# Kernel optimization log

Hardware: AMD Instinct MI355X
Metric: run time of the kernel (lower is better)

Reference implementation:

```python
import jax, jax.numpy as jnp
import numpy as np
import math

N, CIN, DM, H, W = 4, 64, 32, 64, 64
KH = KW = 3

def setup_inputs() -> dict:
    key = jax.random.key(0)
    ks = jax.random.split(key, 12)
    sc = 0.05
    return {
        "h": jax.random.normal(ks[0], (N, CIN, H, W), jnp.float32),
        "m": jax.random.normal(ks[1], (N, CIN, H, W), jnp.float32),
        "Wh": jax.random.normal(ks[2], (3 * DM, CIN), jnp.float32) * sc,
        "bh": jax.random.normal(ks[3], (3 * DM,), jnp.float32) * sc,
        "Wm": jax.random.normal(ks[4], (2 * DM, CIN), jnp.float32) * sc,
        "bm": jax.random.normal(ks[5], (2 * DM,), jnp.float32) * sc,
        "Wz": jax.random.normal(ks[6], (DM, 2 * DM), jnp.float32) * sc,
        "bz": jax.random.normal(ks[7], (DM,), jnp.float32) * sc,
        "Wo": jax.random.normal(ks[8], (3 * CIN, CIN + DM, KH, KW), jnp.float32) * sc,
        "bo": jax.random.normal(ks[9], (3 * CIN,), jnp.float32) * sc,
    }

def _conv1x1(x, Wt, b):
    # x: [N,Ci,H,W], Wt: [Co,Ci] -> [N,Co,H,W]
    return jnp.einsum('oi,nihw->nohw', Wt, x) + b[None, :, None, None]

def _attend(q, k, v):
    # q,k,v: [N,C,S]; out: [N,C,S]
    C = q.shape[1]
    scores = jnp.einsum('ncs,nct->nst', q, k) / math.sqrt(C)  # [N,S,S]
    attn = jax.nn.softmax(scores, axis=-1)
    return jnp.einsum('nst,nct->ncs', attn, v)

def reference(h, m, Wh, bh, Wm, bm, Wz, bz, Wo, bo):
    n, _, hh, ww = h.shape
    S = hh * ww
    hq, hk, hv = jnp.split(_conv1x1(h, Wh, bh), 3, axis=1)
    mk, mv = jnp.split(_conv1x1(m, Wm, bm), 2, axis=1)
    hq = hq.reshape(n, DM, S)
    hk = hk.reshape(n, DM, S)
    hv = hv.reshape(n, DM, S)
    mk = mk.reshape(n, DM, S)
    mv = mv.reshape(n, DM, S)
    Zh = _attend(hq, hk, hv).reshape(n, DM, hh, ww)
    Zm = _attend(hq, mk, mv).reshape(n, DM, hh, ww)
    Z = _conv1x1(jnp.concatenate([Zh, Zm], axis=1), Wz, bz)
    x = jnp.concatenate([Z, h], axis=1)  # [N, DM+CIN, H, W]
    out = jax.lax.conv_general_dilated(
        x, Wo, window_strides=(1, 1), padding='SAME',
        dimension_numbers=('NCHW', 'OIHW', 'NCHW')) + bo[None, :, None, None]
    i, g, o = jnp.split(out, 3, axis=1)
    i = jax.nn.sigmoid(i)
    g = jnp.tanh(g)
    m_next = i * g + (1.0 - i) * m
    h_next = jax.nn.sigmoid(o) * m_next
    return (h_next, m_next)
```

## Files before the change

kernel.cpp:

```cpp
#include <hip/hip_runtime.h>
#include <math.h>

#define NB 4
#define CIN 64
#define DM 32
#define S 4096
#define NW 4

#define OFF_Q  0
#define OFF_KH 262144
#define OFF_VH 524288
#define OFF_KM 786432
#define OFF_VM 1048576
#define OFF_ZH 1310720
#define OFF_ZM 1572864
#define OFF_WF 1835008

typedef __attribute__((ext_vector_type(8))) short bf16x8;
typedef __attribute__((ext_vector_type(4))) short s16x4;
typedef __attribute__((ext_vector_type(4))) float f32x4;
typedef __attribute__((ext_vector_type(2))) unsigned int u32x2;

__device__ inline unsigned short f2b(float x) {
  union { float f; unsigned u; } v;
  v.f = x;
  unsigned r = (v.u + 0x7FFF + ((v.u >> 16) & 1)) >> 16;
  return (unsigned short)r;
}

__device__ inline float b2f(unsigned short u) {
  union { unsigned u; float f; } v;
  v.u = ((unsigned)u) << 16;
  return v.f;
}

__device__ inline unsigned fbits(float x) {
  union { float f; unsigned u; } v;
  v.f = x;
  return v.u;
}

__global__ __launch_bounds__(256) void prep_kernel(
    const float* __restrict__ h, const float* __restrict__ m,
    const float* __restrict__ Wh, const float* __restrict__ bh,
    const float* __restrict__ Wm, const float* __restrict__ bm,
    const float* __restrict__ Wo, float* __restrict__ ws) {
  __shared__ unsigned short sm[64][34];
  int bid = blockIdx.x;
  int tid = threadIdx.x;

  if (bid >= 512) {
    int idx = (bid - 512) * 256 + tid;
    int co = idx / 432;
    int rem = idx - co * 432;
    int tap = rem / 48;
    int cp = rem - tap * 48;
    int ci0 = cp * 2;
    float a = Wo[((size_t)co * 96 + ci0) * 9 + tap];
    float b = Wo[((size_t)co * 96 + ci0 + 1) * 9 + tap];
    unsigned val = (unsigned)f2b(a) | ((unsigned)f2b(b) << 16);
    ((unsigned*)(ws + OFF_WF))[idx] = val;
    return;
  }

  int mode = (bid >= 256) ? 1 : 0;
  const float* in = mode ? m : h;
  const float* W = mode ? Wm : Wh;
  const float* b = mode ? bm : bh;
  int lbid = bid & 255;
  int n = lbid >> 6;
  int s0 = (lbid & 63) * 64;
  int sl = tid & 63;
  int cg = tid >> 6;
  const float* inp = in + (size_t)n * CIN * S + s0 + sl;

  float reg[64];
#pragma unroll
  for (int ci = 0; ci < 64; ++ci) reg[ci] = inp[(size_t)ci * S];

  float acc[24];
  if (mode == 0) {
#pragma unroll
    for (int k = 0; k < 24; ++k) {
      int co = cg + k * 4;
      const float* w = W + co * CIN;
      float a = b[co];
#pragma unroll
      for (int ci = 0; ci < CIN; ++ci) a += w[ci] * reg[ci];
      acc[k] = a;
    }
  } else {
#pragma unroll
    for (int k = 0; k < 16; ++k) {
      int co = cg + k * 4;
      const float* w = W + co * CIN;
      float a = b[co];
#pragma unroll
      for (int ci = 0; ci < CIN; ++ci) a += w[ci] * reg[ci];
      acc[k] = a;
    }
  }

  unsigned short* qsl = (unsigned short*)(ws + OFF_Q);
  unsigned short* khs = (unsigned short*)(ws + OFF_KH);
  unsigned short* vhs = (unsigned short*)(ws + OFF_VH);
  unsigned short* kms = (unsigned short*)(ws + OFF_KM);
  unsigned short* vms = (unsigned short*)(ws + OFF_VM);

  int ngrp = (mode == 0) ? 2 : 1;
  for (int g = 0; g < ngrp; ++g) {
    __syncthreads();
    const float rs = 0.2550400330665387f;
#pragma unroll
    for (int j = 0; j < 8; ++j) {
      int k = g * 8 + j;
      int c = cg + 4 * j;
      float v = acc[k];
      if (mode == 0 && g == 0) v *= rs;
      sm[sl][c] = f2b(v);
    }
    __syncthreads();
    unsigned short* dst;
    if (mode == 0)
      dst = (g == 0 ? qsl : khs);
    else
      dst = kms;
    unsigned* du = (unsigned*)(dst + ((size_t)n * S + s0) * 32);
#pragma unroll
    for (int i = 0; i < 4; ++i) {
      int idx = tid + i * 256;
      int s = idx >> 4, cp = idx & 15;
      unsigned val = (unsigned)sm[s][2 * cp] | ((unsigned)sm[s][2 * cp + 1] << 16);
      du[idx] = val;
    }
  }
  int k0 = (mode == 0) ? 16 : 8;
  unsigned short* vdst = (mode == 0) ? vhs : vms;
#pragma unroll
  for (int j = 0; j < 8; ++j) {
    int k = k0 + j;
    int c = cg + 4 * j;
    vdst[((size_t)n * DM + c) * S + s0 + sl] = f2b(acc[k]);
  }
}

union AttnSmem {
  unsigned short P[NW][2][1024];
  float osh[NW][2][32][16];
};

__global__ __launch_bounds__(256, 4) void attn_kernel(
    float* __restrict__ ws, const float* __restrict__ Wz,
    const float* __restrict__ bz) {
  __shared__ __align__(16) AttnSmem sm;
  __shared__ float lsh[NW][2][16];
  __shared__ unsigned short Olds[2][16][40];

  int bid = blockIdx.x;
  int ph = bid & 1;
  int n = (bid >> 1) & 3;
  int q0 = (bid >> 3) * 32;
  int tid = threadIdx.x;
  int w = tid >> 6;
  int lane = tid & 63;
  int ql = lane & 15;
  int quad = lane >> 4;
  int kbase = w * 1024;
  int sw = 2 * (ql & 7);

  const unsigned short* qs = (const unsigned short*)(ws + OFF_Q) + ((size_t)n * S + q0) * 32;
  const unsigned short* Ks = (const unsigned short*)(ws + (ph ? OFF_KM : OFF_KH)) + (size_t)n * S * 32;
  const unsigned short* Vs = (const unsigned short*)(ws + (ph ? OFF_VM : OFF_VH)) + (size_t)n * DM * S;
  unsigned short* Zp = (unsigned short*)(ws + (ph ? OFF_ZM : OFF_ZH)) + (size_t)n * DM * S;

  bf16x8 qf0 = *(const bf16x8*)(qs + ql * 32 + quad * 8);
  bf16x8 qf1 = *(const bf16x8*)(qs + (16 + ql) * 32 + quad * 8);

  f32x4 o00 = {0.f, 0.f, 0.f, 0.f}, o01 = {0.f, 0.f, 0.f, 0.f};
  f32x4 o10 = {0.f, 0.f, 0.f, 0.f}, o11 = {0.f, 0.f, 0.f, 0.f};
  f32x4 lsv0 = {0.f, 0.f, 0.f, 0.f}, lsv1 = {0.f, 0.f, 0.f, 0.f};
  const float ZI = -11.541560327111707f;
  const f32x4 zinit = {ZI, ZI, ZI, ZI};

  bf16x8 kfa[4], kfb[4];
#pragma unroll
  for (int t = 0; t < 4; ++t)
    kfa[t] = *(const bf16x8*)(Ks + (size_t)(kbase + t * 16 + ql) * 32 + quad * 8);

  auto step = [&](bf16x8 (&kfc)[4], bf16x8 (&kfn)[4], int kb, int kbn) {
    bf16x8 vf[4];
#pragma unroll
    for (int c2 = 0; c2 < 2; ++c2)
#pragma unroll
      for (int t2 = 0; t2 < 2; ++t2)
        vf[c2 * 2 + t2] = *(const bf16x8*)(Vs + (size_t)(t2 * 16 + ql) * S + kb + c2 * 32 + quad * 8);
#pragma unroll
    for (int t = 0; t < 4; ++t)
      kfn[t] = *(const bf16x8*)(Ks + (size_t)(kbn + t * 16 + ql) * 32 + quad * 8);

#pragma unroll
    for (int t = 0; t < 4; ++t) {
      f32x4 stt = __builtin_amdgcn_mfma_f32_16x16x32_bf16(kfc[t], qf0, zinit, 0, 0, 0);
      f32x4 e;
#pragma unroll
      for (int r = 0; r < 4; ++r) e[r] = __builtin_amdgcn_exp2f(stt[r]);
      lsv0 += e;
      u32x2 pk;
      pk[0] = __builtin_amdgcn_perm(fbits(e[1]), fbits(e[0]), 0x07060302u);
      pk[1] = __builtin_amdgcn_perm(fbits(e[3]), fbits(e[2]), 0x07060302u);
      *(u32x2*)(&sm.P[w][0][ql * 64 + ((t * 4 + quad) ^ sw) * 4]) = pk;
    }
#pragma unroll
    for (int t = 0; t < 4; ++t) {
      f32x4 stt = __builtin_amdgcn_mfma_f32_16x16x32_bf16(kfc[t], qf1, zinit, 0, 0, 0);
      f32x4 e;
#pragma unroll
      for (int r = 0; r < 4; ++r) e[r] = __builtin_amdgcn_exp2f(stt[r]);
      lsv1 += e;
      u32x2 pk;
      pk[0] = __builtin_amdgcn_perm(fbits(e[1]), fbits(e[0]), 0x07060302u);
      pk[1] = __builtin_amdgcn_perm(fbits(e[3]), fbits(e[2]), 0x07060302u);
      *(u32x2*)(&sm.P[w][1][ql * 64 + ((t * 4 + quad) ^ sw) * 4]) = pk;
    }

    __builtin_amdgcn_s_waitcnt(0xC07F);
    __builtin_amdgcn_wave_barrier();

#pragma unroll
    for (int c2 = 0; c2 < 2; ++c2) {
      bf16x8 pf0 = *(const bf16x8*)(&sm.P[w][0][ql * 64 + ((c2 * 8 + quad * 2) ^ sw) * 4]);
      bf16x8 pf1 = *(const bf16x8*)(&sm.P[w][1][ql * 64 + ((c2 * 8 + quad * 2) ^ sw) * 4]);
      o00 = __builtin_amdgcn_mfma_f32_16x16x32_bf16(vf[c2 * 2 + 0], pf0, o00, 0, 0, 0);
      o01 = __builtin_amdgcn_mfma_f32_16x16x32_bf16(vf[c2 * 2 + 1], pf0, o01, 0, 0, 0);
      o10 = __builtin_amdgcn_mfma_f32_16x16x32_bf16(vf[c2 * 2 + 0], pf1, o10, 0, 0, 0);
      o11 = __builtin_amdgcn_mfma_f32_16x16x32_bf16(vf[c2 * 2 + 1], pf1, o11, 0, 0, 0);
    }
    __builtin_amdgcn_wave_barrier();
  };

  for (int it = 0; it < 16; it += 2) {
    int kb0 = kbase + it * 64;
    int kb1 = kbase + ((it + 1) & 15) * 64;
    int kb2 = kbase + ((it + 2) & 15) * 64;
    step(kfa, kfb, kb0, kb1);
    step(kfb, kfa, kb1, kb2);
  }

  float lrun0 = lsv0[0] + lsv0[1] + lsv0[2] + lsv0[3];
  float lrun1 = lsv1[0] + lsv1[1] + lsv1[2] + lsv1[3];
  lrun0 += __shfl_xor(lrun0, 16);
  lrun0 += __shfl_xor(lrun0, 32);
  lrun1 += __shfl_xor(lrun1, 16);
  lrun1 += __shfl_xor(lrun1, 32);

  __syncthreads();
#pragma unroll
  for (int r = 0; r < 4; ++r) {
    sm.osh[w][0][quad * 4 + r][ql] = o00[r];
    sm.osh[w][0][16 + quad * 4 + r][ql] = o01[r];
    sm.osh[w][1][quad * 4 + r][ql] = o10[r];
    sm.osh[w][1][16 + quad * 4 + r][ql] = o11[r];
  }
  if (quad == 0) {
    lsh[w][0][ql] = lrun0;
    lsh[w][1][ql] = lrun1;
  }
  __syncthreads();

  if (w < 2) {
    int qt = w;
    float l = 0.f;
    f32x4 a0 = {0.f, 0.f, 0.f, 0.f}, a1 = {0.f, 0.f, 0.f, 0.f};
#pragma unroll
    for (int i = 0; i < NW; ++i) {
      l += lsh[i][qt][ql];
#pragma unroll
      for (int r = 0; r < 4; ++r) {
        a0[r] += sm.osh[i][qt][quad * 4 + r][ql];
        a1[r] += sm.osh[i][qt][16 + quad * 4 + r][ql];
      }
    }
    float inv = 1.0f / l;
    s16x4 w0, w1;
#pragma unroll
    for (int r = 0; r < 4; ++r) {
      w0[r] = (short)f2b(a0[r] * inv);
      w1[r] = (short)f2b(a1[r] * inv);
    }
    *(s16x4*)(&Olds[qt][ql][quad * 4]) = w0;
    *(s16x4*)(&Olds[qt][ql][16 + quad * 4]) = w1;
    __builtin_amdgcn_s_waitcnt(0xC07F);
    __builtin_amdgcn_wave_barrier();
    bf16x8 of = *(const bf16x8*)(&Olds[qt][ql][quad * 8]);

    const float* wzr0 = Wz + (size_t)ql * (2 * DM) + ph * DM + quad * 8;
    const float* wzr1 = Wz + (size_t)(ql + 16) * (2 * DM) + ph * DM + quad * 8;
    bf16x8 a0f, a1f;
#pragma unroll
    for (int j = 0; j < 8; ++j) {
      a0f[j] = (short)f2b(wzr0[j]);
      a1f[j] = (short)f2b(wzr1[j]);
    }
    f32x4 z0 = {0.f, 0.f, 0.f, 0.f}, z1 = {0.f, 0.f, 0.f, 0.f};
    if (ph == 0) {
#pragma unroll
      for (int r = 0; r < 4; ++r) {
        z0[r] = bz[quad * 4 + r];
        z1[r] = bz[16 + quad * 4 + r];
      }
    }
    z0 = __builtin_amdgcn_mfma_f32_16x16x32_bf16(a0f, of, z0, 0, 0, 0);
    z1 = __builtin_amdgcn_mfma_f32_16x16x32_bf16(a1f, of, z1, 0, 0, 0);
    int qc = q0 + qt * 16 + ql;
#pragma unroll
    for (int r = 0; r < 4; ++r) {
      Zp[(size_t)(quad * 4 + r) * S + qc] = f2b(z0[r]);
      Zp[(size_t)(16 + quad * 4 + r) * S + qc] = f2b(z1[r]);
    }
  }
}

__global__ __launch_bounds__(256) void conv_mfma_kernel(
    const float* __restrict__ ws, const float* __restrict__ h,
    const float* __restrict__ m, const float* __restrict__ bo,
    float* __restrict__ out) {
  __shared__ unsigned short xt[3][66][104];
  int bid = blockIdx.x;
  int n = bid >> 7;
  int rem = bid & 127;
  int g = rem & 1;
  int y = rem >> 1;
  int tid = threadIdx.x;
  int wv = tid >> 6;
  int lane = tid & 63;
  int ql = lane & 15, quad = lane >> 4;
  int x0 = wv * 16;

  const unsigned short* Zh = (const unsigned short*)(ws + OFF_ZH) + (size_t)n * DM * S;
  const unsigned short* Zm = (const unsigned short*)(ws + OFF_ZM) + (size_t)n * DM * S;
  const float* hb = h + (size_t)n * CIN * S;
  const unsigned short* Wf = (const unsigned short*)(ws + OFF_WF);

#pragma unroll
  for (int k = 0; k < 36; ++k) {
    int idx = tid + k * 256;
    int xm1 = idx & 63;
    int t2 = idx >> 6;
    int cp = t2 % 48;
    int r3 = t2 / 48;
    int yy = y + r3 - 1;
    unsigned val = 0u;
    if (yy >= 0 && yy < 64) {
      int s = yy * 64 + xm1;
      int ci0 = 2 * cp;
      float a, b;
      if (ci0 < 32) {
        a = b2f(Zh[(size_t)ci0 * S + s]) + b2f(Zm[(size_t)ci0 * S + s]);
        b = b2f(Zh[(size_t)(ci0 + 1) * S + s]) + b2f(Zm[(size_t)(ci0 + 1) * S + s]);
      } else {
        a = hb[(size_t)(ci0 - 32) * S + s];
        b = hb[(size_t)(ci0 - 31) * S + s];
      }
      val = (unsigned)f2b(a) | ((unsigned)f2b(b) << 16);
    }
    *(unsigned*)(&xt[r3][xm1 + 1][2 * cp]) = val;
  }
#pragma unroll
  for (int k = 0; k < 2; ++k) {
    int idx = tid + k * 256;
    if (idx < 288) {
      int r3 = idx / 96;
      int rm = idx % 96;
      int side = rm / 48;
      int cp = rm % 48;
      *(unsigned*)(&xt[r3][side * 65][2 * cp]) = 0u;
    }
  }
  __syncthreads();

  f32x4 acc[6];
#pragma unroll
  for (int t = 0; t < 6; ++t) acc[t] = (f32x4){0.f, 0.f, 0.f, 0.f};

  const unsigned short* wb[6];
#pragma unroll
  for (int j = 0; j < 6; ++j) {
    int cob = (j >> 1) * 64 + g * 32 + (j & 1) * 16;
    wb[j] = Wf + (size_t)(cob + ql) * 864 + quad * 8;
  }

#pragma unroll
  for (int dy = 0; dy < 3; ++dy) {
#pragma unroll
    for (int dx = 0; dx < 3; ++dx) {
      int tap = dy * 3 + dx;
#pragma unroll
      for (int cc = 0; cc < 3; ++cc) {
        bf16x8 b = *(const bf16x8*)(&xt[dy][x0 + ql + dx][cc * 32 + quad * 8]);
        int ko = tap * 96 + cc * 32;
#pragma unroll
        for (int j = 0; j < 6; ++j) {
          bf16x8 wf = *(const bf16x8*)(wb[j] + ko);
          acc[j] = __builtin_amdgcn_mfma_f32_16x16x32_bf16(wf, b, acc[j], 0, 0, 0);
        }
      }
    }
  }

  int s = y * 64 + x0 + ql;
#pragma unroll
  for (int jj = 0; jj < 2; ++jj) {
#pragma unroll
    for (int r = 0; r < 4; ++r) {
      int c = g * 32 + jj * 16 + quad * 4 + r;
      float iv = acc[jj][r] + bo[c];
      float gv = acc[2 + jj][r] + bo[64 + c];
      float ov = acc[4 + jj][r] + bo[128 + c];
      float ig = 1.f / (1.f + __expf(-iv));
      float gg = tanhf(gv);
      float og = 1.f / (1.f + __expf(-ov));
      size_t oidx = (((size_t)n * 64 + c) << 12) + s;
      float mold = m[oidx];
      float mn = ig * gg + (1.f - ig) * mold;
      out[oidx] = og * mn;
      out[(size_t)NB * CIN * S + oidx] = mn;
    }
  }
}

extern "C" void kernel_launch(void* const* d_in, const int* in_sizes, int n_in,
                              void* d_out, int out_size, void* d_ws, size_t ws_size,
                              hipStream_t stream) {
  const float* h = (const float*)d_in[0];
  const float* m = (const float*)d_in[1];
  const float* Wh = (const float*)d_in[2];
  const float* bh = (const float*)d_in[3];
  const float* Wm = (const float*)d_in[4];
  const float* bm = (const float*)d_in[5];
  const float* Wz = (const float*)d_in[6];
  const float* bz = (const float*)d_in[7];
  const float* Wo = (const float*)d_in[8];
  const float* bo = (const float*)d_in[9];
  float* out = (float*)d_out;
  float* ws = (float*)d_ws;

  prep_kernel<<<836, 256, 0, stream>>>(h, m, Wh, bh, Wm, bm, Wo, ws);
  attn_kernel<<<2 * NB * (S / 32), 256, 0, stream>>>(ws, Wz, bz);
  conv_mfma_kernel<<<NB * 128, 256, 0, stream>>>(ws, h, m, bo, out);
}
```

Baseline: 186.4 us.

## Software-pipeline attention loop with double-buffered P tiles across iterations

Restructures the attention inner loop so the QK^T+exp for tile i is computed while the PV MFMAs consume the P tile from tile i-1, using a double-buffered shared-memory P array. V fragments are also double-buffered and loaded one step ahead, with a prologue and epilogue handling the first and last tiles. The goal is to overlap exp/ALU work and LDS round-trips with matrix-core work and remove one wave barrier per step. In exchange it doubles P shared memory and raises register pressure, which may affect occupancy at launch bounds of 4.

```diff
diff --git a/kernel.cpp b/kernel.cpp
--- a/kernel.cpp
+++ b/kernel.cpp
@@ -145,7 +145,7 @@
 }
 
 union AttnSmem {
-  unsigned short P[NW][2][1024];
+  unsigned short P[NW][2][2][1024];
   float osh[NW][2][32][16];
 };
 
@@ -182,22 +182,7 @@
   const float ZI = -11.541560327111707f;
   const f32x4 zinit = {ZI, ZI, ZI, ZI};
 
-  bf16x8 kfa[4], kfb[4];
-#pragma unroll
-  for (int t = 0; t < 4; ++t)
-    kfa[t] = *(const bf16x8*)(Ks + (size_t)(kbase + t * 16 + ql) * 32 + quad * 8);
-
-  auto step = [&](bf16x8 (&kfc)[4], bf16x8 (&kfn)[4], int kb, int kbn) {
-    bf16x8 vf[4];
-#pragma unroll
-    for (int c2 = 0; c2 < 2; ++c2)
-#pragma unroll
-      for (int t2 = 0; t2 < 2; ++t2)
-        vf[c2 * 2 + t2] = *(const bf16x8*)(Vs + (size_t)(t2 * 16 + ql) * S + kb + c2 * 32 + quad * 8);
-#pragma unroll
-    for (int t = 0; t < 4; ++t)
-      kfn[t] = *(const bf16x8*)(Ks + (size_t)(kbn + t * 16 + ql) * 32 + quad * 8);
-
+  auto qkexp = [&](bf16x8(&kfc)[4], int pb) {
 #pragma unroll
     for (int t = 0; t < 4; ++t) {
       f32x4 stt = __builtin_amdgcn_mfma_f32_16x16x32_bf16(kfc[t], qf0, zinit, 0, 0, 0);
@@ -208,7 +193,7 @@
       u32x2 pk;
       pk[0] = __builtin_amdgcn_perm(fbits(e[1]), fbits(e[0]), 0x07060302u);
       pk[1] = __builtin_amdgcn_perm(fbits(e[3]), fbits(e[2]), 0x07060302u);
-      *(u32x2*)(&sm.P[w][0][ql * 64 + ((t * 4 + quad) ^ sw) * 4]) = pk;
+      *(u32x2*)(&sm.P[w][pb][0][ql * 64 + ((t * 4 + quad) ^ sw) * 4]) = pk;
     }
 #pragma unroll
     for (int t = 0; t < 4; ++t) {
@@ -220,30 +205,72 @@
       u32x2 pk;
       pk[0] = __builtin_amdgcn_perm(fbits(e[1]), fbits(e[0]), 0x07060302u);
       pk[1] = __builtin_amdgcn_perm(fbits(e[3]), fbits(e[2]), 0x07060302u);
-      *(u32x2*)(&sm.P[w][1][ql * 64 + ((t * 4 + quad) ^ sw) * 4]) = pk;
-    }
-
+      *(u32x2*)(&sm.P[w][pb][1][ql * 64 + ((t * 4 + quad) ^ sw) * 4]) = pk;
+    }
+  };
+
+  bf16x8 kfa[4], kfb[4], vfa[4], vfb[4];
+#pragma unroll
+  for (int t = 0; t < 4; ++t)
+    kfa[t] = *(const bf16x8*)(Ks + (size_t)(kbase + t * 16 + ql) * 32 + quad * 8);
+#pragma unroll
+  for (int c2 = 0; c2 < 2; ++c2)
+#pragma unroll
+    for (int t2 = 0; t2 < 2; ++t2)
+      vfa[c2 * 2 + t2] = *(const bf16x8*)(Vs + (size_t)(t2 * 16 + ql) * S + kbase + c2 * 32 + quad * 8);
+#pragma unroll
+  for (int t = 0; t < 4; ++t)
+    kfb[t] = *(const bf16x8*)(Ks + (size_t)(kbase + 64 + t * 16 + ql) * 32 + quad * 8);
+  qkexp(kfa, 0);
+
+  auto step = [&](int it, bf16x8(&kfc)[4], bf16x8(&kfn)[4],
+                  bf16x8(&vfp)[4], bf16x8(&vfc)[4]) {
+    int kbc = kbase + it * 64;
+    int kbn = kbase + ((it + 1) & 15) * 64;
+    int pbc = it & 1, pbp = pbc ^ 1;
+#pragma unroll
+    for (int t = 0; t < 4; ++t)
+      kfn[t] = *(const bf16x8*)(Ks + (size_t)(kbn + t * 16 + ql) * 32 + quad * 8);
+#pragma unroll
+    for (int c2 = 0; c2 < 2; ++c2)
+#pragma unroll
+      for (int t2 = 0; t2 < 2; ++t2)
+        vfc[c2 * 2 + t2] = *(const bf16x8*)(Vs + (size_t)(t2 * 16 + ql) * S + kbc + c2 * 32 + quad * 8);
     __builtin_amdgcn_s_waitcnt(0xC07F);
     __builtin_amdgcn_wave_barrier();
-
+    bf16x8 pf[4];
 #pragma unroll
     for (int c2 = 0; c2 < 2; ++c2) {
-      bf16x8 pf0 = *(const bf16x8*)(&sm.P[w][0][ql * 64 + ((c2 * 8 + quad * 2) ^ sw) * 4]);
-      bf16x8 pf1 = *(const bf16x8*)(&sm.P[w][1][ql * 64 + ((c2 * 8 + quad * 2) ^ sw) * 4]);
-      o00 = __builtin_amdgcn_mfma_f32_16x16x32_bf16(vf[c2 * 2 + 0], pf0, o00, 0, 0, 0);
-      o01 = __builtin_amdgcn_mfma_f32_16x16x32_bf16(vf[c2 * 2 + 1], pf0, o01, 0, 0, 0);
-      o10 = __builtin_amdgcn_mfma_f32_16x16x32_bf16(vf[c2 * 2 + 0], pf1, o10, 0, 0, 0);
-      o11 = __builtin_amdgcn_mfma_f32_16x16x32_bf16(vf[c2 * 2 + 1], pf1, o11, 0, 0, 0);
-    }
-    __builtin_amdgcn_wave_barrier();
+      pf[c2] = *(const bf16x8*)(&sm.P[w][pbp][0][ql * 64 + ((c2 * 8 + quad * 2) ^ sw) * 4]);
+      pf[2 + c2] = *(const bf16x8*)(&sm.P[w][pbp][1][ql * 64 + ((c2 * 8 + quad * 2) ^ sw) * 4]);
+    }
+    qkexp(kfc, pbc);
+#pragma unroll
+    for (int c2 = 0; c2 < 2; ++c2) {
+      o00 = __builtin_amdgcn_mfma_f32_16x16x32_bf16(vfp[c2 * 2 + 0], pf[c2], o00, 0, 0, 0);
+      o01 = __builtin_amdgcn_mfma_f32_16x16x32_bf16(vfp[c2 * 2 + 1], pf[c2], o01, 0, 0, 0);
+      o10 = __builtin_amdgcn_mfma_f32_16x16x32_bf16(vfp[c2 * 2 + 0], pf[2 + c2], o10, 0, 0, 0);
+      o11 = __builtin_amdgcn_mfma_f32_16x16x32_bf16(vfp[c2 * 2 + 1], pf[2 + c2], o11, 0, 0, 0);
+    }
   };
 
-  for (int it = 0; it < 16; it += 2) {
-    int kb0 = kbase + it * 64;
-    int kb1 = kbase + ((it + 1) & 15) * 64;
-    int kb2 = kbase + ((it + 2) & 15) * 64;
-    step(kfa, kfb, kb0, kb1);
-    step(kfb, kfa, kb1, kb2);
+  step(1, kfb, kfa, vfa, vfb);
+#pragma unroll 1
+  for (int it = 2; it < 16; it += 2) {
+    step(it, kfa, kfb, vfb, vfa);
+    step(it + 1, kfb, kfa, vfa, vfb);
+  }
+
+  __builtin_amdgcn_s_waitcnt(0xC07F);
+  __builtin_amdgcn_wave_barrier();
+#pragma unroll
+  for (int c2 = 0; c2 < 2; ++c2) {
+    bf16x8 pf0 = *(const bf16x8*)(&sm.P[w][1][0][ql * 64 + ((c2 * 8 + quad * 2) ^ sw) * 4]);
+    bf16x8 pf1 = *(const bf16x8*)(&sm.P[w][1][1][ql * 64 + ((c2 * 8 + quad * 2) ^ sw) * 4]);
+    o00 = __builtin_amdgcn_mfma_f32_16x16x32_bf16(vfb[c2 * 2 + 0], pf0, o00, 0, 0, 0);
+    o01 = __builtin_amdgcn_mfma_f32_16x16x32_bf16(vfb[c2 * 2 + 1], pf0, o01, 0, 0, 0);
+    o10 = __builtin_amdgcn_mfma_f32_16x16x32_bf16(vfb[c2 * 2 + 0], pf1, o10, 0, 0, 0);
+    o11 = __builtin_amdgcn_mfma_f32_16x16x32_bf16(vfb[c2 * 2 + 1], pf1, o11, 0, 0, 0);
   }
 
   float lrun0 = lsv0[0] + lsv0[1] + lsv0[2] + lsv0[3];
```

After: 219.4 us. 1.18x slower.
